# Optimization experiments

Hardware: AMD Instinct MI355X
Metric: run time of the kernel (lower is better)

Reference implementation:

```python
import jax, jax.numpy as jnp
import numpy as np

N_NODES = 50000
N_EDGES = 800000
F_IN = 24
H = 128
N_GRAPHS = 100
BN_EPS = 1e-5


def setup_inputs() -> dict:
    key = jax.random.key(0)
    ks = jax.random.split(key, 12)
    x = jax.random.normal(ks[0], (N_NODES, F_IN), dtype=jnp.float32)
    edge_index = jax.random.randint(ks[1], (2, N_EDGES), 0, N_NODES, dtype=jnp.int32)
    batch = (jnp.arange(N_NODES, dtype=jnp.int32) // (N_NODES // N_GRAPHS)).astype(jnp.int32)

    def lin(k, fan_in, fan_out):
        bound = 1.0 / np.sqrt(fan_in)
        kw, kb = jax.random.split(k)
        W = jax.random.uniform(kw, (fan_in, fan_out), jnp.float32, -bound, bound)
        b = jax.random.uniform(kb, (fan_out,), jnp.float32, -bound, bound)
        return W, b

    W1, b1 = lin(ks[2], 2 * F_IN, H)
    W2, b2 = lin(ks[3], 2 * H, H)
    W3, b3 = lin(ks[4], 2 * H, H)
    Wl, bl = lin(ks[5], H, 1)
    g1 = jnp.ones((H,), jnp.float32); be1 = jnp.zeros((H,), jnp.float32)
    g2 = jnp.ones((H,), jnp.float32); be2 = jnp.zeros((H,), jnp.float32)
    g3 = jnp.ones((H,), jnp.float32); be3 = jnp.zeros((H,), jnp.float32)
    return {"x": x, "edge_index": edge_index, "batch": batch,
            "W1": W1, "b1": b1, "W2": W2, "b2": b2, "W3": W3, "b3": b3,
            "g1": g1, "be1": be1, "g2": g2, "be2": be2, "g3": g3, "be3": be3,
            "Wl": Wl, "bl": bl}


def edge_conv(x, src, dst, W, b):
    # PyG EdgeConv: message = mlp([x_i, x_j - x_i]) for edge j->i, aggr=max at i
    x_i = x[dst]                                    # [E, F]
    e = jnp.concatenate([x_i, x[src] - x_i], axis=-1)  # [E, 2F]
    m = jax.nn.relu(e @ W + b)                      # [E, H]
    out = jax.ops.segment_max(m, dst, num_segments=N_NODES)
    return jnp.where(jnp.isfinite(out), out, 0.0)   # isolated nodes -> 0


def batch_norm(h, g, b):
    # training-mode BN over node dim (biased variance), dropout treated as identity
    mu = h.mean(axis=0)
    var = ((h - mu) ** 2).mean(axis=0)
    return g * (h - mu) * jax.lax.rsqrt(var + BN_EPS) + b


def reference(x, edge_index, batch, W1, b1, W2, b2, W3, b3,
              g1, be1, g2, be2, g3, be3, Wl, bl):
    src, dst = edge_index[0], edge_index[1]
    h = edge_conv(x, src, dst, W1, b1)
    h = jax.nn.relu(batch_norm(h, g1, be1))
    h = edge_conv(h, src, dst, W2, b2)
    h = jax.nn.relu(batch_norm(h, g2, be2))
    h = edge_conv(h, src, dst, W3, b3)
    h = batch_norm(h, g3, be3)
    # global_mean_pool
    sums = jax.ops.segment_sum(h, batch, num_segments=N_GRAPHS)           # [G, H]
    counts = jax.ops.segment_sum(jnp.ones((h.shape[0],), h.dtype), batch,
                                 num_segments=N_GRAPHS)
    pooled = sums / jnp.maximum(counts, 1.0)[:, None]
    return jax.nn.relu(pooled @ Wl + bl)                                  # [G, 1]
```

## Files before the change

### kernel.cpp

```cpp
#include <hip/hip_runtime.h>

#define N_NODES 50000
#define N_EDGES 800000
#define F_IN 24
#define HDIM 128
#define N_GRAPHS 100
#define BN_EPS 1e-5f
#define NBLK 196
#define ROWS_PER_GRAPH (N_NODES / N_GRAPHS)
#define MM_GRID 782
#define HIST_BLKS ((N_EDGES + 255) / 256)
#define PREP_BLKS (F_IN + 2 * HDIM)
#define SSTR 32
#define SUMS_PER_LAYER (256 * SSTR)

typedef _Float16 h2 __attribute__((ext_vector_type(2)));
typedef _Float16 f16x8 __attribute__((ext_vector_type(8)));
typedef float f32x4 __attribute__((ext_vector_type(4)));

template <int K, int KC>
__global__ __launch_bounds__(256) void k_mm1(const float* __restrict__ X,
                                             const float* __restrict__ Wcat,
                                             const float* __restrict__ bias,
                                             float* __restrict__ A, _Float16* __restrict__ C) {
    __shared__ float Xs[KC * 68];
    __shared__ float Ws[KC * 128];
    int tid = threadIdx.x;
    int row0 = blockIdx.x * 64;
    const bool isA = (blockIdx.y == 0);
    const int colbase = isA ? 0 : 128;
    int cg = tid & 31;
    int rg = tid >> 5;

    float acc[8][4];
#pragma unroll
    for (int ri = 0; ri < 8; ++ri)
#pragma unroll
        for (int ci = 0; ci < 4; ++ci)
            acc[ri][ci] = isA ? bias[cg * 4 + ci] : 0.f;

    for (int k0 = 0; k0 < K; k0 += KC) {
        __syncthreads();
        {
            const int C4 = KC / 4;
            for (int i = tid; i < 64 * C4; i += 256) {
                int c4 = i % C4, r = i / C4;
                int row = row0 + r;
                float4 v = make_float4(0.f, 0.f, 0.f, 0.f);
                if (row < N_NODES) v = *(const float4*)&X[row * K + k0 + c4 * 4];
                Xs[(c4 * 4 + 0) * 68 + r] = v.x;
                Xs[(c4 * 4 + 1) * 68 + r] = v.y;
                Xs[(c4 * 4 + 2) * 68 + r] = v.z;
                Xs[(c4 * 4 + 3) * 68 + r] = v.w;
            }
        }
        for (int i = tid; i < KC * 32; i += 256) {
            int c4 = i & 31, kr = i >> 5;
            *(float4*)&Ws[kr * 128 + c4 * 4] =
                *(const float4*)&Wcat[(k0 + kr) * 256 + colbase + c4 * 4];
        }
        __syncthreads();
#pragma unroll
        for (int kk = 0; kk < KC; ++kk) {
            float4 t0 = *(const float4*)&Xs[kk * 68 + rg * 8];
            float4 t1 = *(const float4*)&Xs[kk * 68 + rg * 8 + 4];
            float4 w = *(const float4*)&Ws[kk * 128 + cg * 4];
            float t[8] = {t0.x, t0.y, t0.z, t0.w, t1.x, t1.y, t1.z, t1.w};
            float wv[4] = {w.x, w.y, w.z, w.w};
#pragma unroll
            for (int ri = 0; ri < 8; ++ri)
#pragma unroll
                for (int ci = 0; ci < 4; ++ci)
                    acc[ri][ci] += t[ri] * wv[ci];
        }
    }

#pragma unroll
    for (int ri = 0; ri < 8; ++ri) {
        int row = row0 + rg * 8 + ri;
        if (row < N_NODES) {
            if (isA) {
                *(float4*)&A[row * HDIM + cg * 4] =
                    make_float4(acc[ri][0], acc[ri][1], acc[ri][2], acc[ri][3]);
            } else {
                union { h2 h[2]; uint2 u; } pk;
                pk.h[0] = h2{(_Float16)acc[ri][0], (_Float16)acc[ri][1]};
                pk.h[1] = h2{(_Float16)acc[ri][2], (_Float16)acc[ri][3]};
                *(uint2*)&C[row * HDIM + cg * 4] = pk.u;
            }
        }
    }
}

__global__ __launch_bounds__(256) void k_mmf(const float* __restrict__ X,
                                             const _Float16* __restrict__ Wf,
                                             const float* __restrict__ bias,
                                             const float* __restrict__ sums,
                                             const float* __restrict__ g,
                                             const float* __restrict__ be,
                                             float* __restrict__ A, _Float16* __restrict__ C) {
    __shared__ _Float16 Xh[16 * 520];
    __shared__ _Float16 Wh[128 * 128];
    __shared__ float scs[128], shs[128];
    int tid = threadIdx.x;
    int lane = tid & 63, wv = tid >> 6;
    int row0 = blockIdx.x * 64;
    const bool isA = (blockIdx.y == 0);
    const _Float16* Wsrc = Wf + (isA ? 0 : 16384);

    if (tid < 128) {
        float S  = sums[tid * SSTR];
        float S2 = sums[(128 + tid) * SSTR];
        float mean = S / (float)N_NODES;
        float var = fmaxf(S2 / (float)N_NODES - mean * mean, 0.f);
        float scv = g[tid] / sqrtf(var + BN_EPS);
        scs[tid] = scv;
        shs[tid] = be[tid] - mean * scv;
    }
    {
        const uint4* s = (const uint4*)Wsrc;
        uint4* d = (uint4*)Wh;
        for (int i = tid; i < 2048; i += 256) d[i] = s[i];
    }
    __syncthreads();
    for (int i = tid; i < 64 * 32; i += 256) {
        int k4 = i & 31, rl = i >> 5;
        int row = row0 + rl;
        float4 v = make_float4(0.f, 0.f, 0.f, 0.f);
        if (row < N_NODES) v = *(const float4*)&X[row * HDIM + k4 * 4];
        int c = k4 * 4;
        v.x = fmaxf(v.x * scs[c + 0] + shs[c + 0], 0.f);
        v.y = fmaxf(v.y * scs[c + 1] + shs[c + 1], 0.f);
        v.z = fmaxf(v.z * scs[c + 2] + shs[c + 2], 0.f);
        v.w = fmaxf(v.w * scs[c + 3] + shs[c + 3], 0.f);
        int rt = rl >> 4, m = rl & 15, kc = k4 >> 3, q = (k4 >> 1) & 3, jh = k4 & 1;
        _Float16* d = Xh + (rt * 4 + kc) * 520 + (q * 16 + m) * 8 + jh * 4;
        d[0] = (_Float16)v.x; d[1] = (_Float16)v.y;
        d[2] = (_Float16)v.z; d[3] = (_Float16)v.w;
    }
    __syncthreads();

    int n = lane & 15, q = lane >> 4;
    f32x4 acc[8];
#pragma unroll
    for (int nt = 0; nt < 8; ++nt) {
        float b0 = isA ? bias[nt * 16 + n] : 0.f;
        acc[nt] = f32x4{b0, b0, b0, b0};
    }
#pragma unroll
    for (int kc = 0; kc < 4; ++kc) {
        f16x8 a = *(const f16x8*)(Xh + (wv * 4 + kc) * 520 + lane * 8);
#pragma unroll
        for (int nt = 0; nt < 8; ++nt) {
            f16x8 b = *(const f16x8*)(Wh + ((nt * 4 + kc) * 64 + lane) * 8);
            acc[nt] = __builtin_amdgcn_mfma_f32_16x16x32_f16(a, b, acc[nt], 0, 0, 0);
        }
    }
#pragma unroll
    for (int nt = 0; nt < 8; ++nt) {
#pragma unroll
        for (int r = 0; r < 4; ++r) {
            int row = row0 + wv * 16 + q * 4 + r;
            if (row < N_NODES) {
                int col = nt * 16 + n;
                if (isA) A[row * HDIM + col] = acc[nt][r];
                else     C[row * HDIM + col] = (_Float16)acc[nt][r];
            }
        }
    }
}

__global__ void k_pre(const float* __restrict__ W1, const float* __restrict__ W2,
                      const float* __restrict__ W3, float* __restrict__ Wcat1,
                      _Float16* __restrict__ Wf2, _Float16* __restrict__ Wf3,
                      const int* __restrict__ dst, unsigned* __restrict__ deg,
                      unsigned* __restrict__ rank) {
    int b = blockIdx.x;
    int j = threadIdx.x;
    if (b < F_IN) {
        float wb = W1[(b + F_IN) * HDIM + (j & 127)];
        float wt = W1[b * HDIM + (j & 127)];
        Wcat1[b * 256 + j] = (j < HDIM) ? (wt - wb) : wb;
    } else if (b < PREP_BLKS) {
        int idx = b - F_IN;
        int layer = idx >> 7;
        int k = idx & 127;
        const float* W = layer ? W3 : W2;
        _Float16* Wf   = layer ? Wf3 : Wf2;
        int col = j & 127;
        float wt = W[k * HDIM + col];
        float wb = W[(k + HDIM) * HDIM + col];
        float v = (j < 128) ? (wt - wb) : wb;
        int plane = j >> 7;
        int nt = col >> 4, n = col & 15, kc = k >> 5, q = (k >> 3) & 3, jj = k & 7;
        int f = ((nt * 4 + kc) * 4 + q) * 128 + n * 8 + jj;
        Wf[plane * 16384 + f] = (_Float16)v;
    } else {
        int e = (b - PREP_BLKS) * 256 + j;
        if (e < N_EDGES) rank[e] = atomicAdd(&deg[dst[e]], 1u);
    }
}

__global__ __launch_bounds__(256) void k_scanall(const unsigned* __restrict__ deg,
                                                 unsigned* __restrict__ bsum,
                                                 unsigned* __restrict__ off) {
    __shared__ unsigned s[256];
    int t = threadIdx.x;
    int b = blockIdx.x;
    int i = b * 256 + t;
    unsigned v = (i < N_NODES) ? deg[i] : 0u;
    s[t] = v;
    __syncthreads();
    for (int d = 1; d < 256; d <<= 1) {
        unsigned u = (t >= d) ? s[t - d] : 0u;
        __syncthreads();
        s[t] += u;
        __syncthreads();
    }
    unsigned locex = s[t] - v;
    if (t == 255) atomicExch(&bsum[b], s[255] + 1u);
    __syncthreads();
    unsigned bs = 0;
    if (t < NBLK) {
        unsigned x;
        do { x = atomicAdd(&bsum[t], 0u); } while (x == 0u);
        bs = x - 1u;
    }
    s[t] = (t < NBLK) ? bs : 0u;
    __syncthreads();
    for (int d = 1; d < 256; d <<= 1) {
        unsigned u = (t >= d) ? s[t - d] : 0u;
        __syncthreads();
        s[t] += u;
        __syncthreads();
    }
    unsigned bexcl = (b == 0) ? 0u : s[b - 1];
    if (i < N_NODES) off[i] = bexcl + locex;
}

__global__ void k_scatter(const int* __restrict__ src, const int* __restrict__ dst,
                          const unsigned* __restrict__ off, const unsigned* __restrict__ rank,
                          unsigned* __restrict__ ssrc) {
    int e = blockIdx.x * 256 + threadIdx.x;
    if (e < N_EDGES)
        ssrc[off[dst[e]] + rank[e]] = (unsigned)src[e];
}

__global__ __launch_bounds__(256) void k_agg(const float* __restrict__ A,
                                             const h2* __restrict__ Cc,
                                             const unsigned* __restrict__ off,
                                             const unsigned* __restrict__ deg,
                                             const unsigned* __restrict__ ssrc,
                                             float* __restrict__ H) {
    __shared__ unsigned sl[4][64];
    int w = threadIdx.x >> 6;
    int lane = threadIdx.x & 63;
    int i = blockIdx.x * 4 + w;
    int d = (int)deg[i];
    unsigned o = off[i];
    union { unsigned short us[2]; h2 v; } ninf;
    ninf.us[0] = 0xFC00; ninf.us[1] = 0xFC00;
    h2 m2 = ninf.v;
    for (int base = 0; base < d; base += 64) {
        int cntc = min(64, d - base);
        if (lane < cntc) sl[w][lane] = ssrc[o + base + lane];
        int e = 0;
        for (; e + 8 <= cntc; e += 8) {
            unsigned s0 = sl[w][e + 0], s1 = sl[w][e + 1], s2 = sl[w][e + 2], s3 = sl[w][e + 3];
            unsigned s4 = sl[w][e + 4], s5 = sl[w][e + 5], s6 = sl[w][e + 6], s7 = sl[w][e + 7];
            h2 v0 = Cc[s0 * 64 + lane];
            h2 v1 = Cc[s1 * 64 + lane];
            h2 v2 = Cc[s2 * 64 + lane];
            h2 v3 = Cc[s3 * 64 + lane];
            h2 v4 = Cc[s4 * 64 + lane];
            h2 v5 = Cc[s5 * 64 + lane];
            h2 v6 = Cc[s6 * 64 + lane];
            h2 v7 = Cc[s7 * 64 + lane];
            h2 a0 = __builtin_elementwise_max(v0, v1);
            h2 a1 = __builtin_elementwise_max(v2, v3);
            h2 a2 = __builtin_elementwise_max(v4, v5);
            h2 a3 = __builtin_elementwise_max(v6, v7);
            h2 b0 = __builtin_elementwise_max(a0, a1);
            h2 b1 = __builtin_elementwise_max(a2, a3);
            m2 = __builtin_elementwise_max(m2, __builtin_elementwise_max(b0, b1));
        }
        if (e + 4 <= cntc) {
            unsigned s0 = sl[w][e + 0], s1 = sl[w][e + 1], s2 = sl[w][e + 2], s3 = sl[w][e + 3];
            h2 v0 = Cc[s0 * 64 + lane];
            h2 v1 = Cc[s1 * 64 + lane];
            h2 v2 = Cc[s2 * 64 + lane];
            h2 v3 = Cc[s3 * 64 + lane];
            h2 a0 = __builtin_elementwise_max(v0, v1);
            h2 a1 = __builtin_elementwise_max(v2, v3);
            m2 = __builtin_elementwise_max(m2, __builtin_elementwise_max(a0, a1));
            e += 4;
        }
        for (; e < cntc; ++e)
            m2 = __builtin_elementwise_max(m2, Cc[sl[w][e] * 64 + lane]);
    }
    float2 a = *(const float2*)&A[i * HDIM + lane * 2];
    float2 hv;
    hv.x = (d > 0) ? fmaxf(a.x + (float)m2.x, 0.f) : 0.f;
    hv.y = (d > 0) ? fmaxf(a.y + (float)m2.y, 0.f) : 0.f;
    *(float2*)&H[i * HDIM + lane * 2] = hv;
}

__global__ __launch_bounds__(256) void k_stats(const float* __restrict__ H,
                                               float* __restrict__ sums) {
    __shared__ float4 ls[256], ls2[256];
    int t = threadIdx.x;
    int c4 = t & 31, rg = t >> 5;
    int row0 = blockIdx.x * 64;
    float4 s = make_float4(0.f, 0.f, 0.f, 0.f);
    float4 s2 = make_float4(0.f, 0.f, 0.f, 0.f);
#pragma unroll
    for (int it = 0; it < 8; ++it) {
        int row = row0 + rg * 8 + it;
        if (row < N_NODES) {
            float4 v = *(const float4*)&H[row * HDIM + c4 * 4];
            s.x += v.x; s.y += v.y; s.z += v.z; s.w += v.w;
            s2.x += v.x * v.x; s2.y += v.y * v.y; s2.z += v.z * v.z; s2.w += v.w * v.w;
        }
    }
    ls[t] = s; ls2[t] = s2;
    __syncthreads();
    if (t < 32) {
        float4 a = ls[t], a2 = ls2[t];
#pragma unroll
        for (int j = 1; j < 8; ++j) {
            float4 b = ls[j * 32 + t], b2 = ls2[j * 32 + t];
            a.x += b.x; a.y += b.y; a.z += b.z; a.w += b.w;
            a2.x += b2.x; a2.y += b2.y; a2.z += b2.z; a2.w += b2.w;
        }
        int c = t * 4;
        atomicAdd(&sums[(c + 0) * SSTR], a.x);
        atomicAdd(&sums[(c + 1) * SSTR], a.y);
        atomicAdd(&sums[(c + 2) * SSTR], a.z);
        atomicAdd(&sums[(c + 3) * SSTR], a.w);
        atomicAdd(&sums[(128 + c + 0) * SSTR], a2.x);
        atomicAdd(&sums[(128 + c + 1) * SSTR], a2.y);
        atomicAdd(&sums[(128 + c + 2) * SSTR], a2.z);
        atomicAdd(&sums[(128 + c + 3) * SSTR], a2.w);
    }
}

__global__ __launch_bounds__(128) void k_poolout(const float* __restrict__ H,
                                                 const float* __restrict__ sums,
                                                 const float* __restrict__ g,
                                                 const float* __restrict__ be,
                                                 const float* __restrict__ Wl,
                                                 const float* __restrict__ bl,
                                                 float* __restrict__ out) {
    int gi = blockIdx.x;
    int k = threadIdx.x;
    float S  = sums[k * SSTR];
    float S2 = sums[(128 + k) * SSTR];
    float mean = S / (float)N_NODES;
    float var = fmaxf(S2 / (float)N_NODES - mean * mean, 0.f);
    float scv = g[k] / sqrtf(var + BN_EPS);
    float shv = be[k] - mean * scv;
    const float* base = H + (size_t)gi * ROWS_PER_GRAPH * HDIM;
    float s = 0.f;
#pragma unroll 4
    for (int r = 0; r < ROWS_PER_GRAPH; ++r) s += base[r * HDIM + k];
    float pb = scv * (s * (1.f / (float)ROWS_PER_GRAPH)) + shv;
    float p = pb * Wl[k];
    __shared__ float red[2];
    for (int o = 32; o > 0; o >>= 1) p += __shfl_down(p, o);
    if ((k & 63) == 0) red[k >> 6] = p;
    __syncthreads();
    if (k == 0) out[gi] = fmaxf(red[0] + red[1] + bl[0], 0.f);
}

extern "C" void kernel_launch(void* const* d_in, const int* in_sizes, int n_in,
                              void* d_out, int out_size, void* d_ws, size_t ws_size,
                              hipStream_t stream) {
    const float* x   = (const float*)d_in[0];
    const int* ei    = (const int*)d_in[1];
    const float* W1  = (const float*)d_in[3];
    const float* b1  = (const float*)d_in[4];
    const float* W2  = (const float*)d_in[5];
    const float* b2  = (const float*)d_in[6];
    const float* W3  = (const float*)d_in[7];
    const float* b3  = (const float*)d_in[8];
    const float* g1  = (const float*)d_in[9];
    const float* be1 = (const float*)d_in[10];
    const float* g2  = (const float*)d_in[11];
    const float* be2 = (const float*)d_in[12];
    const float* g3  = (const float*)d_in[13];
    const float* be3 = (const float*)d_in[14];
    const float* Wl  = (const float*)d_in[15];
    const float* bl  = (const float*)d_in[16];
    float* out = (float*)d_out;

    const int* srcp = ei;
    const int* dstp = ei + N_EDGES;

    char* ws = (char*)d_ws;
    size_t o = 0;
    auto alloc = [&](size_t bytes) -> void* {
        o = (o + 255) & ~(size_t)255;
        void* p = ws + o;
        o += bytes;
        return p;
    };
    float* A      = (float*)alloc((size_t)N_NODES * HDIM * 4);
    _Float16* C   = (_Float16*)alloc((size_t)N_NODES * HDIM * 2);
    float* h      = (float*)alloc((size_t)N_NODES * HDIM * 4);
    float* Wcat1  = (float*)alloc((size_t)F_IN * 256 * 4);
    _Float16* Wf2 = (_Float16*)alloc((size_t)2 * 16384 * 2);
    _Float16* Wf3 = (_Float16*)alloc((size_t)2 * 16384 * 2);
    unsigned* deg  = (unsigned*)alloc((size_t)N_NODES * 4);
    unsigned* bsum = (unsigned*)alloc((size_t)NBLK * 4);
    float* sums    = (float*)alloc((size_t)3 * SUMS_PER_LAYER * 4);
    unsigned* off  = (unsigned*)alloc((size_t)N_NODES * 4);
    unsigned* rank = (unsigned*)alloc((size_t)N_EDGES * 4);
    unsigned* ssrc = (unsigned*)alloc((size_t)N_EDGES * 4);
    (void)ws_size; (void)n_in; (void)in_sizes; (void)out_size;

    float* sums0 = sums;
    float* sums1 = sums + SUMS_PER_LAYER;
    float* sums2 = sums + 2 * SUMS_PER_LAYER;

    size_t zlen = (size_t)((char*)(sums + 3 * SUMS_PER_LAYER) - (char*)deg);
    (void)hipMemsetAsync(deg, 0, zlen, stream);

    k_pre<<<PREP_BLKS + HIST_BLKS, 256, 0, stream>>>(W1, W2, W3, Wcat1, Wf2, Wf3,
                                                     dstp, deg, rank);
    k_scanall<<<NBLK, 256, 0, stream>>>(deg, bsum, off);
    k_scatter<<<HIST_BLKS, 256, 0, stream>>>(srcp, dstp, off, rank, ssrc);

    const dim3 MMG(MM_GRID, 2);
    const int AGB = N_NODES / 4;

    k_mm1<F_IN, F_IN><<<MMG, 256, 0, stream>>>(x, Wcat1, b1, A, C);
    k_agg<<<AGB, 256, 0, stream>>>(A, (const h2*)C, off, deg, ssrc, h);
    k_stats<<<MM_GRID, 256, 0, stream>>>(h, sums0);

    k_mmf<<<MMG, 256, 0, stream>>>(h, Wf2, b2, sums0, g1, be1, A, C);
    k_agg<<<AGB, 256, 0, stream>>>(A, (const h2*)C, off, deg, ssrc, h);
    k_stats<<<MM_GRID, 256, 0, stream>>>(h, sums1);

    k_mmf<<<MMG, 256, 0, stream>>>(h, Wf3, b3, sums1, g2, be2, A, C);
    k_agg<<<AGB, 256, 0, stream>>>(A, (const h2*)C, off, deg, ssrc, h);
    k_stats<<<MM_GRID, 256, 0, stream>>>(h, sums2);

    k_poolout<<<N_GRAPHS, 128, 0, stream>>>(h, sums2, g3, be3, Wl, bl, out);
}
```

Measured before the change: 424.5 us.

## Partition edge gathers in aggregation kernel into source-node slabs

The max-aggregation kernel now splits each node's neighbour list into 8 source-index slabs using wave ballots and processes one slab at a time. The aim is to improve L2/cache locality of the random fp16 row gathers, assuming concurrently running waves touch similar slabs. It adds 8 ballot/compaction passes per chunk and splits the unrolled gather loops into shorter runs, which reduces memory-level parallelism per wave. Nothing synchronises the waves across the GPU, so they may not actually work on the same slab at the same time.

```diff
diff --git a/kernel.cpp b/kernel.cpp
--- a/kernel.cpp
+++ b/kernel.cpp
@@ -13,6 +13,8 @@
 #define PREP_BLKS (F_IN + 2 * HDIM)
 #define SSTR 32
 #define SUMS_PER_LAYER (256 * SSTR)
+#define SLABS 8
+#define SLAB_SZ (N_NODES / SLABS)
 
 typedef _Float16 h2 __attribute__((ext_vector_type(2)));
 typedef _Float16 f16x8 __attribute__((ext_vector_type(8)));
@@ -252,7 +254,7 @@
                                              const unsigned* __restrict__ deg,
                                              const unsigned* __restrict__ ssrc,
                                              float* __restrict__ H) {
-    __shared__ unsigned sl[4][64];
+    __shared__ unsigned slc[4][64];
     int w = threadIdx.x >> 6;
     int lane = threadIdx.x & 63;
     int i = blockIdx.x * 4 + w;
@@ -263,40 +265,51 @@
     h2 m2 = ninf.v;
     for (int base = 0; base < d; base += 64) {
         int cntc = min(64, d - base);
-        if (lane < cntc) sl[w][lane] = ssrc[o + base + lane];
-        int e = 0;
-        for (; e + 8 <= cntc; e += 8) {
-            unsigned s0 = sl[w][e + 0], s1 = sl[w][e + 1], s2 = sl[w][e + 2], s3 = sl[w][e + 3];
-            unsigned s4 = sl[w][e + 4], s5 = sl[w][e + 5], s6 = sl[w][e + 6], s7 = sl[w][e + 7];
-            h2 v0 = Cc[s0 * 64 + lane];
-            h2 v1 = Cc[s1 * 64 + lane];
-            h2 v2 = Cc[s2 * 64 + lane];
-            h2 v3 = Cc[s3 * 64 + lane];
-            h2 v4 = Cc[s4 * 64 + lane];
-            h2 v5 = Cc[s5 * 64 + lane];
-            h2 v6 = Cc[s6 * 64 + lane];
-            h2 v7 = Cc[s7 * 64 + lane];
-            h2 a0 = __builtin_elementwise_max(v0, v1);
-            h2 a1 = __builtin_elementwise_max(v2, v3);
-            h2 a2 = __builtin_elementwise_max(v4, v5);
-            h2 a3 = __builtin_elementwise_max(v6, v7);
-            h2 b0 = __builtin_elementwise_max(a0, a1);
-            h2 b1 = __builtin_elementwise_max(a2, a3);
-            m2 = __builtin_elementwise_max(m2, __builtin_elementwise_max(b0, b1));
-        }
-        if (e + 4 <= cntc) {
-            unsigned s0 = sl[w][e + 0], s1 = sl[w][e + 1], s2 = sl[w][e + 2], s3 = sl[w][e + 3];
-            h2 v0 = Cc[s0 * 64 + lane];
-            h2 v1 = Cc[s1 * 64 + lane];
-            h2 v2 = Cc[s2 * 64 + lane];
-            h2 v3 = Cc[s3 * 64 + lane];
-            h2 a0 = __builtin_elementwise_max(v0, v1);
-            h2 a1 = __builtin_elementwise_max(v2, v3);
-            m2 = __builtin_elementwise_max(m2, __builtin_elementwise_max(a0, a1));
-            e += 4;
-        }
-        for (; e < cntc; ++e)
-            m2 = __builtin_elementwise_max(m2, Cc[sl[w][e] * 64 + lane]);
+        unsigned sv = 0xFFFFFFFFu;
+        if (lane < cntc) sv = ssrc[o + base + lane];
+#pragma unroll 1
+        for (int slab = 0; slab < SLABS; ++slab) {
+            unsigned lo = (unsigned)(slab * SLAB_SZ);
+            bool cond = (sv - lo) < (unsigned)SLAB_SZ;
+            unsigned long long mask = __ballot(cond);
+            int cnt = __popcll(mask);
+            if (cnt == 0) continue;
+            int pos = __popcll(mask & ((1ull << lane) - 1ull));
+            if (cond) slc[w][pos] = sv;
+            int e = 0;
+            for (; e + 8 <= cnt; e += 8) {
+                unsigned s0 = slc[w][e + 0], s1 = slc[w][e + 1], s2 = slc[w][e + 2], s3 = slc[w][e + 3];
+                unsigned s4 = slc[w][e + 4], s5 = slc[w][e + 5], s6 = slc[w][e + 6], s7 = slc[w][e + 7];
+                h2 v0 = Cc[s0 * 64 + lane];
+                h2 v1 = Cc[s1 * 64 + lane];
+                h2 v2 = Cc[s2 * 64 + lane];
+                h2 v3 = Cc[s3 * 64 + lane];
+                h2 v4 = Cc[s4 * 64 + lane];
+                h2 v5 = Cc[s5 * 64 + lane];
+                h2 v6 = Cc[s6 * 64 + lane];
+                h2 v7 = Cc[s7 * 64 + lane];
+                h2 a0 = __builtin_elementwise_max(v0, v1);
+                h2 a1 = __builtin_elementwise_max(v2, v3);
+                h2 a2 = __builtin_elementwise_max(v4, v5);
+                h2 a3 = __builtin_elementwise_max(v6, v7);
+                h2 b0 = __builtin_elementwise_max(a0, a1);
+                h2 b1 = __builtin_elementwise_max(a2, a3);
+                m2 = __builtin_elementwise_max(m2, __builtin_elementwise_max(b0, b1));
+            }
+            if (e + 4 <= cnt) {
+                unsigned s0 = slc[w][e + 0], s1 = slc[w][e + 1], s2 = slc[w][e + 2], s3 = slc[w][e + 3];
+                h2 v0 = Cc[s0 * 64 + lane];
+                h2 v1 = Cc[s1 * 64 + lane];
+                h2 v2 = Cc[s2 * 64 + lane];
+                h2 v3 = Cc[s3 * 64 + lane];
+                h2 a0 = __builtin_elementwise_max(v0, v1);
+                h2 a1 = __builtin_elementwise_max(v2, v3);
+                m2 = __builtin_elementwise_max(m2, __builtin_elementwise_max(a0, a1));
+                e += 4;
+            }
+            for (; e < cnt; ++e)
+                m2 = __builtin_elementwise_max(m2, Cc[slc[w][e] * 64 + lane]);
+        }
     }
     float2 a = *(const float2*)&A[i * HDIM + lane * 2];
     float2 hv;
```

Result: slower. 480.0 us (+13.1%).
